# Kernel tuning notes

Measured on AMD Instinct MI355X. Metric: run time of the kernel, lower is better.

## Reference

```python
import jax, jax.numpy as jnp
import numpy as np

B, TC, TT, E, V = 512, 64, 16, 512, 256
E2 = E // 2


def entmax15(z):
    # exact sort-based 1.5-entmax over last axis (Peters et al., 2019)
    z = z / 2.0
    z = z - jnp.max(z, axis=-1, keepdims=True)  # shift-invariant, for stability
    z_srt = -jnp.sort(-z, axis=-1)
    d = z.shape[-1]
    rho = jnp.arange(1, d + 1, dtype=z.dtype)
    mean = jnp.cumsum(z_srt, axis=-1) / rho
    mean_sq = jnp.cumsum(z_srt * z_srt, axis=-1) / rho
    ss = rho * (mean_sq - mean * mean)
    delta = (1.0 - ss) / rho
    pos = delta > 0
    sqrt_d = jnp.where(pos, jnp.sqrt(jnp.where(pos, delta, 1.0)), 0.0)
    tau = mean - sqrt_d
    k = jnp.sum((tau <= z_srt).astype(jnp.int32), axis=-1, keepdims=True)
    tau_star = jnp.take_along_axis(tau, k - 1, axis=-1)
    y = jnp.clip(z - tau_star, 0.0)
    return y * y


def _mha(q_seq, kv, wq, wk, wv, bq, bk, bv, wo, bo):
    # single-head attention; q_seq: (T,B,E) decoder states, kv: (B,S,E) encoder memory
    e = q_seq.shape[-1]
    q = (q_seq @ wq.T + bq) * (1.0 / jnp.sqrt(jnp.asarray(e, q_seq.dtype)))
    k = kv @ wk.T + bk
    v = kv @ wv.T + bv
    a = jax.nn.softmax(jnp.einsum('tbe,bse->bts', q, k), axis=-1)
    o = jnp.einsum('bts,bse->tbe', a, v)
    return o @ wo.T + bo


def setup_inputs() -> dict:
    key = jax.random.key(0)
    ks = jax.random.split(key, 20)
    rn = lambda k, s, sc=1.0: sc * jax.random.normal(k, s, dtype=jnp.float32)
    z = lambda s: jnp.zeros(s, jnp.float32)
    return {
        'char_encoding': rn(ks[0], (B, TC, E)),
        'char_hn0': rn(ks[1], (B, E2)),
        'char_cn0': rn(ks[2], (B, E2)),
        'tag_encoding': rn(ks[3], (B, TT, E)),
        'tag_hn0': rn(ks[4], (B, E2)),
        'tag_cn0': rn(ks[5], (B, E2)),
        'true_output_seq': jax.random.uniform(ks[6], (B, TC, V), dtype=jnp.float32),
        'w_ih': rn(ks[7], (4 * E, V), 0.05),
        'w_hh': rn(ks[8], (4 * E, E), 0.05),
        'b_ih': z((4 * E,)),
        'b_hh': z((4 * E,)),
        'char_wq': rn(ks[9], (E, E), 0.05), 'char_wk': rn(ks[10], (E, E), 0.05), 'char_wv': rn(ks[11], (E, E), 0.05),
        'char_bq': z((E,)), 'char_bk': z((E,)), 'char_bv': z((E,)),
        'char_wo': rn(ks[12], (E, E), 0.05), 'char_bo': z((E,)),
        'tag_wq': rn(ks[13], (E, E), 0.05), 'tag_wk': rn(ks[14], (E, E), 0.05), 'tag_wv': rn(ks[15], (E, E), 0.05),
        'tag_bq': z((E,)), 'tag_bk': z((E,)), 'tag_bv': z((E,)),
        'tag_wo': rn(ks[16], (E, E), 0.05), 'tag_bo': z((E,)),
        'out_w': rn(ks[17], (V, 2 * E), 0.05),
        'out_b': z((V,)),
    }


def reference(char_encoding, char_hn0, char_cn0, tag_encoding, tag_hn0, tag_cn0, true_output_seq, w_ih, w_hh, b_ih, b_hh, char_wq, char_wk, char_wv, char_bq, char_bk, char_bv, char_wo, char_bo, tag_wq, tag_wk, tag_wv, tag_bq, tag_bk, tag_bv, tag_wo, tag_bo, out_w, out_b):
    # initial cell state = concat of the two encoders' final (h, c)
    h0 = jnp.concatenate([char_hn0, tag_hn0], axis=-1)
    c0 = jnp.concatenate([char_cn0, tag_cn0], axis=-1)
    # teacher forcing: input at t=0 is zeros, then true_output_seq[:, t]
    xs = jnp.concatenate([jnp.zeros_like(true_output_seq[:, :1]), true_output_seq[:, 1:]], axis=1)
    xs = jnp.swapaxes(xs, 0, 1)  # (T, B, V)

    def cell(carry, x):
        h, c = carry
        gates = x @ w_ih.T + b_ih + h @ w_hh.T + b_hh
        i, f, g, o = jnp.split(gates, 4, axis=-1)  # torch gate order i,f,g,o
        c = jax.nn.sigmoid(f) * c + jax.nn.sigmoid(i) * jnp.tanh(g)
        h = jax.nn.sigmoid(o) * jnp.tanh(c)
        return (h, c), h

    _, hs = jax.lax.scan(cell, (h0, c0), xs)  # (T, B, E)
    # attention queries only depend on per-step h, so batch all T queries at once
    ca = _mha(hs, char_encoding, char_wq, char_wk, char_wv, char_bq, char_bk, char_bv, char_wo, char_bo)
    ta = _mha(hs, tag_encoding, tag_wq, tag_wk, tag_wv, tag_bq, tag_bk, tag_bv, tag_wo, tag_bo)
    logits = jnp.concatenate([ca, ta], axis=-1) @ out_w.T + out_b  # (T, B, V)
    return jnp.swapaxes(entmax15(logits), 0, 1)  # (B, T, V)
```

## Files before the change

kernel.cpp:

```cpp
#include <hip/hip_runtime.h>

typedef unsigned short us;
typedef unsigned int u32;
typedef unsigned long long u64;
typedef __bf16 bf16x8 __attribute__((ext_vector_type(8)));
typedef float f32x4 __attribute__((ext_vector_type(4)));

#define MFMA(a,b,c) __builtin_amdgcn_mfma_f32_16x16x32_bf16(a,b,c,0,0,0)

__device__ __forceinline__ us f2bf(float f){
  u32 u = __builtin_bit_cast(u32, f);
  u += 0x7fffu + ((u>>16)&1u);
  return (us)(u>>16);
}
__device__ __forceinline__ float bf2f(us h){
  u32 u = ((u32)h)<<16;
  return __builtin_bit_cast(float, u);
}
__device__ __forceinline__ float sigf(float x){ return 1.0f/(1.0f+__expf(-x)); }
__device__ __forceinline__ float tanh_(float x){ float e=__expf(2.0f*x); return 1.0f - 2.0f/(e+1.0f); }


__global__ void k_prep_wperm(const float* __restrict__ w_hh, const float* __restrict__ w_ih,
                             const float* __restrict__ b_ih, const float* __restrict__ b_hh,
                             us* __restrict__ Wp, float* __restrict__ biasc){
  int n = blockIdx.x; int c = threadIdx.x;
  float v = (c < 512) ? w_hh[(size_t)n*512 + c] : w_ih[(size_t)n*256 + (c-512)];
  int g = n >> 9, eg = n & 511, eb = eg >> 4, ln = eg & 15;
  int kc = c >> 5, qd = (c >> 3) & 3, i = c & 7;
  size_t dst = ((((size_t)eb*24 + kc)*4 + g)*64 + (size_t)(qd*16 + ln))*8 + i;
  Wp[dst] = f2bf(v);
  if (c == 0) biasc[n] = b_ih[n] + b_hh[n];
}

__global__ void k_prep_state(const float* __restrict__ ch, const float* __restrict__ th,
                             const float* __restrict__ cc, const float* __restrict__ tc,
                             us* __restrict__ h0, float* __restrict__ c0){
  int i = blockIdx.x*256 + threadIdx.x;
  int b = i>>9, e = i&511;
  float hv = (e<256)? ch[b*256+e] : th[b*256+e-256];
  float cv = (e<256)? cc[b*256+e] : tc[b*256+e-256];
  h0[i] = f2bf(hv); c0[i] = cv;
}

__global__ void k_xprep(const float* __restrict__ x, us* __restrict__ xbf){
  int g = blockIdx.x*256 + threadIdx.x;
  int v0 = (g & 31) * 8;
  int b  = (g >> 5) & 511;
  int t  = g >> 14;
  const float4* src = (const float4*)(x + ((size_t)(b*64 + t))*256 + v0);
  float4 f0 = src[0], f1 = src[1];
  uint4 pk;
  pk.x = (u32)f2bf(f0.x) | ((u32)f2bf(f0.y)<<16);
  pk.y = (u32)f2bf(f0.z) | ((u32)f2bf(f0.w)<<16);
  pk.z = (u32)f2bf(f1.x) | ((u32)f2bf(f1.y)<<16);
  pk.w = (u32)f2bf(f1.z) | ((u32)f2bf(f1.w)<<16);
  *(uint4*)(xbf + ((size_t)t*512 + b)*256 + v0) = pk;
}

__global__ void k_uvec(const float* __restrict__ bq, const float* __restrict__ wk,
                       float* __restrict__ u){
  int j = blockIdx.x*128 + threadIdx.x;
  float a = 0.f;
  for (int e=0;e<512;++e) a += bq[e]*wk[(size_t)e*512 + j];
  u[j] = a;
}

__global__ void k_pvec(const float* __restrict__ wo, const float* __restrict__ bv,
                       const float* __restrict__ bo, float* __restrict__ p){
  int i = blockIdx.x*128 + threadIdx.x;
  float a = bo[i];
  for (int j=0;j<512;++j) a += wo[(size_t)i*512+j]*bv[j];
  p[i] = a;
}

__global__ void k_bc(const float* __restrict__ out_w, const float* __restrict__ pc,
                     const float* __restrict__ pt, const float* __restrict__ out_b,
                     float* __restrict__ bc){
  int v = threadIdx.x;
  float a = out_b[v];
  for (int i=0;i<512;++i) a += out_w[(size_t)v*1024+i]*pc[i];
  for (int i=0;i<512;++i) a += out_w[(size_t)v*1024+512+i]*pt[i];
  bc[v] = a;
}

template<bool TA, int OMODE>
__global__ __launch_bounds__(256) void k_pgemm(const float* __restrict__ A, int lda,
    const float* __restrict__ B, int ldb, void* C1, void* C2, int ldc, int K){
  __shared__ us As[64][40];
  __shared__ us Bs[64][40];
  int tid=threadIdx.x, w=tid>>6, lane=tid&63, qd=lane>>4, ln=lane&15;
  int m0 = blockIdx.x*64, n0 = blockIdx.y*64;
  f32x4 acc[4] = {};
  for (int kc=0; kc<K/32; ++kc){
    int k0 = kc*32;
    if (!TA){
      int r=tid>>2, c=(tid&3)*8;
      const float* ap = A + (size_t)(m0+r)*lda + k0 + c;
      float4 f0=*(const float4*)ap, f1=*(const float4*)(ap+4);
      uint4 pk;
      pk.x=(u32)f2bf(f0.x)|((u32)f2bf(f0.y)<<16);
      pk.y=(u32)f2bf(f0.z)|((u32)f2bf(f0.w)<<16);
      pk.z=(u32)f2bf(f1.x)|((u32)f2bf(f1.y)<<16);
      pk.w=(u32)f2bf(f1.z)|((u32)f2bf(f1.w)<<16);
      *(uint4*)&As[r][c] = pk;
    } else {
      int kk=tid>>3, mp=(tid&7)*8;
      const float* ap = A + (size_t)(k0+kk)*lda + m0 + mp;
      #pragma unroll
      for (int i=0;i<8;++i) As[mp+i][kk] = f2bf(ap[i]);
    }
    { int kk=tid>>3, np=(tid&7)*8;
      const float* bp = B + (size_t)(k0+kk)*ldb + n0 + np;
      #pragma unroll
      for (int i=0;i<8;++i) Bs[np+i][kk] = f2bf(bp[i]);
    }
    __syncthreads();
    bf16x8 a = *(const bf16x8*)&As[16*w+ln][qd*8];
    #pragma unroll
    for (int j=0;j<4;++j){
      bf16x8 bb = *(const bf16x8*)&Bs[16*j+ln][qd*8];
      acc[j] = MFMA(a, bb, acc[j]);
    }
    __syncthreads();
  }
  #pragma unroll
  for (int j=0;j<4;++j){
    #pragma unroll
    for (int r=0;r<4;++r){
      size_t idx = (size_t)(m0+16*w+qd*4+r)*ldc + (n0+16*j+ln);
      float v = acc[j][r];
      if (OMODE==0) ((float*)C1)[idx] = v;
      else if (OMODE==1) ((us*)C1)[idx] = f2bf(v);
      else {
        us h = f2bf(v);
        ((us*)C1)[idx] = h;
        ((us*)C2)[idx] = f2bf(v - bf2f(h));
      }
    }
  }
}

__global__ __launch_bounds__(256, 1) void k_lstm_all(
    const us* __restrict__ h0, const us* __restrict__ xbf,
    const us* __restrict__ Wp, const float* __restrict__ biasc,
    const float* __restrict__ c0, us* __restrict__ hs,
    unsigned* __restrict__ bars){
  extern __shared__ us Wf[];
  int tid = threadIdx.x, w = tid>>6, lane = tid&63, qd = lane>>4, ln = lane&15;
  int bb = blockIdx.x & 7, eb = blockIdx.x >> 3;
  int b0 = bb*64, e0 = eb*16;
  {
    const uint4* src = (const uint4*)(Wp + (size_t)eb*49152);
    uint4* dst = (uint4*)Wf;
    #pragma unroll
    for (int i=0;i<24;++i) dst[tid + 256*i] = src[tid + 256*i];
  }
  int bA = b0 + 16*w + ln;
  int bC = b0 + 16*w + qd*4;
  int e  = e0 + ln;
  float bias_[4], c_[4];
  #pragma unroll
  for (int j=0;j<4;++j) bias_[j] = biasc[j*512 + e];
  #pragma unroll
  for (int r=0;r<4;++r) c_[r] = c0[(size_t)(bC+r)*512 + e];
  __syncthreads();
  unsigned* flags = bars + (size_t)bb*512;
  unsigned* myflag = flags + eb*16;
  const unsigned* pollp = flags + (lane&31)*16;
  f32x4 xacc[4] = {};
  for (int t=0; t<64; ++t){
    if (t > 0){
      unsigned tgt = (unsigned)t;
      while (true){
        unsigned v = __hip_atomic_load(pollp, __ATOMIC_RELAXED, __HIP_MEMORY_SCOPE_AGENT);
        if (__all((int)(v >= tgt))) break;
        __builtin_amdgcn_s_sleep(1);
      }
    }
    bf16x8 afr[16];
    if (t == 0){
      const us* hrow = h0 + (size_t)bA*512;
      #pragma unroll
      for (int kc=0; kc<16; ++kc)
        afr[kc] = *(const bf16x8*)(hrow + kc*32 + qd*8);
    } else {
      const u64* hq = (const u64*)(hs + ((size_t)bA*64 + (t-1))*512);
      u64 q0[16], q1[16];
      #pragma unroll
      for (int kc=0; kc<16; ++kc){
        q0[kc] = __hip_atomic_load(hq + kc*8 + qd*2 + 0, __ATOMIC_RELAXED, __HIP_MEMORY_SCOPE_AGENT);
        q1[kc] = __hip_atomic_load(hq + kc*8 + qd*2 + 1, __ATOMIC_RELAXED, __HIP_MEMORY_SCOPE_AGENT);
      }
      #pragma unroll
      for (int kc=0; kc<16; ++kc){
        union { u64 q[2]; bf16x8 v; } u_;
        u_.q[0] = q0[kc]; u_.q[1] = q1[kc];
        afr[kc] = u_.v;
      }
    }
    f32x4 acc[4] = {xacc[0], xacc[1], xacc[2], xacc[3]};
    #pragma unroll
    for (int kc=0; kc<16; ++kc){
      #pragma unroll
      for (int j=0;j<4;++j){
        bf16x8 bfrag = *(const bf16x8*)&Wf[(size_t)((kc*4+j)*64 + lane)*8];
        acc[j] = MFMA(afr[kc], bfrag, acc[j]);
      }
    }
    us hb[4];
    #pragma unroll
    for (int r=0;r<4;++r){
      float iv = acc[0][r]+bias_[0], fv = acc[1][r]+bias_[1];
      float gv = acc[2][r]+bias_[2], ov = acc[3][r]+bias_[3];
      float cc2 = sigf(fv)*c_[r] + sigf(iv)*tanh_(gv);
      c_[r] = cc2;
      hb[r] = f2bf(sigf(ov)*tanh_(cc2));
    }
    #pragma unroll
    for (int r=0;r<4;++r){
      u32 v = hb[r];
      u32 p = v | (((u32)__shfl_xor((int)v, 1)) << 16);
      u64 q = (u64)p | (((u64)(u32)__shfl_xor((int)p, 2)) << 32);
      if ((lane & 3) == 0){
        size_t idx = ((size_t)(bC+r)*64 + t)*512 + e0 + ln;
        __hip_atomic_store((u64*)(hs + idx), q, __ATOMIC_RELAXED, __HIP_MEMORY_SCOPE_AGENT);
      }
    }
    if (t < 63){
      __syncthreads();
      if (tid == 0)
        __hip_atomic_store(myflag, (unsigned)(t+1), __ATOMIC_RELAXED, __HIP_MEMORY_SCOPE_AGENT);
      const us* xrow = xbf + ((size_t)(t+1)*512 + bA)*256;
      f32x4 xa[4] = {};
      #pragma unroll
      for (int kx=0; kx<8; ++kx){
        bf16x8 xf = *(const bf16x8*)(xrow + kx*32 + qd*8);
        #pragma unroll
        for (int j=0;j<4;++j){
          bf16x8 bfrag = *(const bf16x8*)&Wf[(size_t)(((16+kx)*4+j)*64 + lane)*8];
          xa[j] = MFMA(xf, bfrag, xa[j]);
        }
      }
      #pragma unroll
      for (int j=0;j<4;++j) xacc[j] = xa[j];
    }
  }
}

__global__ __launch_bounds__(256) void k_gemm(
    const us* __restrict__ Ap, const us* __restrict__ W,
    const float* __restrict__ bias, float alpha, us* __restrict__ C){
  __shared__ us As[128][40];
  __shared__ us Ws[128][40];
  int tid = threadIdx.x; int w = tid>>6; int lane=tid&63;
  int qd=lane>>4, ln=lane&15;
  int m0 = blockIdx.x*128, n0 = blockIdx.y*128;
  int wm = (w&1)*64, wn=(w>>1)*64;
  f32x4 acc[4][4] = {};
  int row = tid>>1; int cp = (tid&1)*16;
  for (int kc=0;kc<16;++kc){
    int k0=kc*32;
    { const uint4* ap = (const uint4*)(Ap + (size_t)(m0+row)*512 + k0+cp);
      *(uint4*)&As[row][cp]=ap[0]; *(uint4*)&As[row][cp+8]=ap[1];
    }
    { const uint4* wp = (const uint4*)(W + (size_t)(n0+row)*512 + k0+cp);
      *(uint4*)&Ws[row][cp]=wp[0]; *(uint4*)&Ws[row][cp+8]=wp[1];
    }
    __syncthreads();
    bf16x8 af[4], bfr[4];
    #pragma unroll
    for (int i=0;i<4;++i) af[i]  = *(const bf16x8*)&As[wm+16*i+ln][qd*8];
    #pragma unroll
    for (int j=0;j<4;++j) bfr[j] = *(const bf16x8*)&Ws[wn+16*j+ln][qd*8];
    #pragma unroll
    for (int i=0;i<4;++i)
      #pragma unroll
      for (int j=0;j<4;++j) acc[i][j]=MFMA(af[i],bfr[j],acc[i][j]);
    __syncthreads();
  }
  #pragma unroll
  for (int j=0;j<4;++j){
    int col = n0+wn+16*j+ln;
    float bv = bias[col];
    #pragma unroll
    for (int i=0;i<4;++i){
      #pragma unroll
      for (int r=0;r<4;++r){
        int rm = m0+wm+16*i+qd*4+r;
        C[(size_t)rm*512 + col] = f2bf(alpha*(acc[i][j][r]+bv));
      }
    }
  }
}

template<int S>
struct alignas(16) ASmem3 {
  static constexpr int SP  = (S<32)?32:S;
  static constexpr int SPp = SP+8;
  us Pbh[64][SPp];
  us Pbl[64][SPp];
  union {
    us Es[S][72];
    struct { us Eh[64][72]; us El[64][72]; } t;
  } u;
  us Ph[64][72];
  us Pl[64][72];
};

template<int S, bool ACC>
__global__ __launch_bounds__(256) void k_attn3(const us* __restrict__ hGp,
    const float* __restrict__ enc, const us* __restrict__ Mvh,
    const us* __restrict__ Mvl, float* __restrict__ out){
  constexpr int NJ  = S/16;
  constexpr int KC2 = ((S<32)?32:S)/32;
  extern __shared__ char smraw[];
  ASmem3<S>& sm = *reinterpret_cast<ASmem3<S>*>(smraw);
  int b = blockIdx.x;
  int tid=threadIdx.x, w=tid>>6, lane=tid&63, qd=lane>>4, ln=lane&15;

  f32x4 sacc[NJ];
  #pragma unroll
  for (int j=0;j<NJ;++j) sacc[j] = (f32x4){0.f,0.f,0.f,0.f};
  const us* hrow = hGp + ((size_t)(b*64 + 16*w + ln))*512;
  for (int ec=0; ec<8; ++ec){
    int e0 = ec*64;
    { int s = tid>>2, ep=(tid&3)*16;
      if (S==64 || tid < 4*S){
        const float* ap = enc + ((size_t)b*S + s)*512 + e0 + ep;
        float4 f0=*(const float4*)ap, f1=*(const float4*)(ap+4);
        float4 f2=*(const float4*)(ap+8), f3=*(const float4*)(ap+12);
        float fv[16]={f0.x,f0.y,f0.z,f0.w,f1.x,f1.y,f1.z,f1.w,
                      f2.x,f2.y,f2.z,f2.w,f3.x,f3.y,f3.z,f3.w};
        u32 pk[8];
        #pragma unroll
        for (int i=0;i<8;++i)
          pk[i] = (u32)f2bf(fv[2*i]) | ((u32)f2bf(fv[2*i+1])<<16);
        uint4* d = (uint4*)&sm.u.Es[s][ep];
        d[0] = make_uint4(pk[0],pk[1],pk[2],pk[3]);
        d[1] = make_uint4(pk[4],pk[5],pk[6],pk[7]);
      }
    }
    __syncthreads();
    #pragma unroll
    for (int kcl=0;kcl<2;++kcl){
      bf16x8 a = *(const bf16x8*)(hrow + e0 + kcl*32 + qd*8);
      #pragma unroll
      for (int j=0;j<NJ;++j){
        bf16x8 bb = *(const bf16x8*)&sm.u.Es[16*j+ln][kcl*32+qd*8];
        sacc[j] = MFMA(a, bb, sacc[j]);
      }
    }
    __syncthreads();
  }

  #pragma unroll
  for (int r=0;r<4;++r){
    float m = sacc[0][r];
    #pragma unroll
    for (int j=1;j<NJ;++j) m = fmaxf(m, sacc[j][r]);
    #pragma unroll
    for (int dl=1; dl<16; dl<<=1) m = fmaxf(m, __shfl_xor(m, dl));
    float ssum = 0.f;
    #pragma unroll
    for (int j=0;j<NJ;++j){ float e_=__expf(sacc[j][r]-m); sacc[j][r]=e_; ssum+=e_; }
    #pragma unroll
    for (int dl=1; dl<16; dl<<=1) ssum += __shfl_xor(ssum, dl);
    float inv = 1.0f/ssum;
    int R = 16*w + qd*4 + r;
    #pragma unroll
    for (int j=0;j<NJ;++j){
      float pv = sacc[j][r]*inv;
      us h = f2bf(pv);
      sm.Pbh[R][16*j+ln] = h;
      sm.Pbl[R][16*j+ln] = f2bf(pv - bf2f(h));
    }
    if (S==16){ sm.Pbh[R][16+ln]=0; sm.Pbl[R][16+ln]=0; }
  }

  f32x4 Lacc[4][4] = {};
  for (int ec=0; ec<8; ++ec){
    int e0 = ec*64;
    { int s = tid>>2, ep=(tid&3)*16;
      if (S==64 || tid < 4*S){
        const float* ap = enc + ((size_t)b*S + s)*512 + e0 + ep;
        float4 f0=*(const float4*)ap, f1=*(const float4*)(ap+4);
        float4 f2=*(const float4*)(ap+8), f3=*(const float4*)(ap+12);
        float fv[16]={f0.x,f0.y,f0.z,f0.w,f1.x,f1.y,f1.z,f1.w,
                      f2.x,f2.y,f2.z,f2.w,f3.x,f3.y,f3.z,f3.w};
        #pragma unroll
        for (int i=0;i<16;++i){
          float v = fv[i]; us h = f2bf(v);
          sm.u.t.Eh[ep+i][s] = h;
          sm.u.t.El[ep+i][s] = f2bf(v - bf2f(h));
        }
      } else if (S==16 && tid < 128){
        int s2 = 16 + ((tid-64)>>2);
        #pragma unroll
        for (int i=0;i<16;++i){ sm.u.t.Eh[ep+i][s2]=0; sm.u.t.El[ep+i][s2]=0; }
      }
    }
    __syncthreads();
    f32x4 pacc[4] = {};
    #pragma unroll
    for (int kcl=0;kcl<KC2;++kcl){
      bf16x8 ah = *(const bf16x8*)&sm.Pbh[16*w+ln][kcl*32+qd*8];
      bf16x8 al = *(const bf16x8*)&sm.Pbl[16*w+ln][kcl*32+qd*8];
      #pragma unroll
      for (int j=0;j<4;++j){
        bf16x8 bh = *(const bf16x8*)&sm.u.t.Eh[16*j+ln][kcl*32+qd*8];
        bf16x8 bl = *(const bf16x8*)&sm.u.t.El[16*j+ln][kcl*32+qd*8];
        pacc[j] = MFMA(ah, bh, pacc[j]);
        pacc[j] = MFMA(ah, bl, pacc[j]);
        pacc[j] = MFMA(al, bh, pacc[j]);
      }
    }
    #pragma unroll
    for (int j=0;j<4;++j)
      #pragma unroll
      for (int r=0;r<4;++r){
        float v = pacc[j][r]; us h = f2bf(v);
        sm.Ph[16*w+qd*4+r][16*j+ln] = h;
        sm.Pl[16*w+qd*4+r][16*j+ln] = f2bf(v - bf2f(h));
      }
    __syncthreads();
    #pragma unroll
    for (int kcl=0;kcl<2;++kcl){
      bf16x8 ah[4], al[4];
      #pragma unroll
      for (int i=0;i<4;++i){
        ah[i] = *(const bf16x8*)&sm.Ph[16*i+ln][kcl*32+qd*8];
        al[i] = *(const bf16x8*)&sm.Pl[16*i+ln][kcl*32+qd*8];
      }
      #pragma unroll
      for (int j=0;j<4;++j){
        int v = 64*w + 16*j + ln;
        bf16x8 mh = *(const bf16x8*)(Mvh + (size_t)v*512 + e0 + kcl*32 + qd*8);
        bf16x8 ml = *(const bf16x8*)(Mvl + (size_t)v*512 + e0 + kcl*32 + qd*8);
        #pragma unroll
        for (int i=0;i<4;++i){
          Lacc[i][j] = MFMA(ah[i], mh, Lacc[i][j]);
          Lacc[i][j] = MFMA(ah[i], ml, Lacc[i][j]);
          Lacc[i][j] = MFMA(al[i], mh, Lacc[i][j]);
        }
      }
    }
  }
  #pragma unroll
  for (int i=0;i<4;++i){
    #pragma unroll
    for (int j=0;j<4;++j){
      int v = 64*w + 16*j + ln;
      #pragma unroll
      for (int r=0;r<4;++r){
        size_t addr = ((size_t)b*64 + 16*i + qd*4 + r)*256 + v;
        if (ACC) out[addr] += Lacc[i][j][r];
        else     out[addr]  = Lacc[i][j][r];
      }
    }
  }
}

__global__ __launch_bounds__(256) void k_entmax(float* __restrict__ out,
                                                const float* __restrict__ bc){
  int tid=threadIdx.x; int w=tid>>6; int lane=tid&63;
  float4 bcv = *(const float4*)(bc + lane*4);
  int base = blockIdx.x*16 + w*4;
  for (int i=0;i<4;++i){
    int row = base + i;
    float* rp = out + (size_t)row*256 + lane*4;
    float4 d = *(const float4*)rp;
    float z[4] = {0.5f*(d.x+bcv.x), 0.5f*(d.y+bcv.y), 0.5f*(d.z+bcv.z), 0.5f*(d.w+bcv.w)};
    float m = fmaxf(fmaxf(z[0],z[1]), fmaxf(z[2],z[3]));
    #pragma unroll
    for (int dl=1; dl<64; dl<<=1) m = fmaxf(m, __shfl_xor(m, dl));
    #pragma unroll
    for (int k=0;k<4;++k) z[k] -= m;
    float tau = -1.0f;
    for (int it=0; it<14; ++it){
      float s1=0.f, s2=0.f;
      #pragma unroll
      for (int k=0;k<4;++k){
        float dd = z[k]-tau; dd = fmaxf(dd, 0.f);
        s1 += dd; s2 += dd*dd;
      }
      #pragma unroll
      for (int dl=1; dl<64; dl<<=1){ s1 += __shfl_xor(s1, dl); s2 += __shfl_xor(s2, dl); }
      tau += (s2 - 1.0f) / (2.0f*fmaxf(s1, 1e-12f));
    }
    float4 y;
    { float dd;
      dd = fmaxf(z[0]-tau,0.f); y.x = dd*dd;
      dd = fmaxf(z[1]-tau,0.f); y.y = dd*dd;
      dd = fmaxf(z[2]-tau,0.f); y.z = dd*dd;
      dd = fmaxf(z[3]-tau,0.f); y.w = dd*dd;
    }
    *(float4*)rp = y;
  }
}


extern "C" void kernel_launch(void* const* d_in, const int* in_sizes, int n_in,
                              void* d_out, int out_size, void* d_ws, size_t ws_size,
                              hipStream_t stream){
  (void)in_sizes; (void)n_in; (void)out_size; (void)ws_size;
  const float* char_enc = (const float*)d_in[0];
  const float* char_hn0 = (const float*)d_in[1];
  const float* char_cn0 = (const float*)d_in[2];
  const float* tag_enc  = (const float*)d_in[3];
  const float* tag_hn0  = (const float*)d_in[4];
  const float* tag_cn0  = (const float*)d_in[5];
  const float* true_out = (const float*)d_in[6];
  const float* w_ih = (const float*)d_in[7];
  const float* w_hh = (const float*)d_in[8];
  const float* b_ih = (const float*)d_in[9];
  const float* b_hh = (const float*)d_in[10];
  const float* c_wq = (const float*)d_in[11];
  const float* c_wk = (const float*)d_in[12];
  const float* c_wv = (const float*)d_in[13];
  const float* c_bq = (const float*)d_in[14];
  const float* c_bv = (const float*)d_in[16];
  const float* c_wo = (const float*)d_in[17];
  const float* c_bo = (const float*)d_in[18];
  const float* t_wq = (const float*)d_in[19];
  const float* t_wk = (const float*)d_in[20];
  const float* t_wv = (const float*)d_in[21];
  const float* t_bq = (const float*)d_in[22];
  const float* t_bv = (const float*)d_in[24];
  const float* t_wo = (const float*)d_in[25];
  const float* t_bo = (const float*)d_in[26];
  const float* out_w = (const float*)d_in[27];
  const float* out_b = (const float*)d_in[28];
  float* out = (float*)d_out;

  char* base = (char*)d_ws;
  char* regA = base;
  us*    Wp    = (us*)   (regA + 0);
  float* biasc = (float*)(regA + 3145728);
  us*    h0    = (us*)   (regA + 3153920);
  float* cst   = (float*)(regA + 3678208);
  float* M1f   = (float*)(regA + 4726784);
  float* M2f   = (float*)(regA + 5251072);
  us*    xbf   = (us*)   (regA + 5775360);
  us*    hG    = (us*)   regA;
  char* regB = base + 33554432;
  us*    Gc_w  = (us*)(regB + 0);
  us*    Gt_w  = (us*)(regB + 524288);
  us*    M1vh  = (us*)(regB + 1048576);
  us*    M1vl  = (us*)(regB + 1310720);
  us*    M2vh  = (us*)(regB + 1572864);
  us*    M2vl  = (us*)(regB + 1835008);
  float* u_c   = (float*)(regB + 2097152);
  float* u_t   = (float*)(regB + 2099200);
  float* p_c   = (float*)(regB + 2101248);
  float* p_t   = (float*)(regB + 2103296);
  float* bc    = (float*)(regB + 2105344);
  us*    hs    = (us*)(base + 33554432 + 2106368);
  unsigned* bars = (unsigned*)(base + 33554432 + 2106368 + 33554432);

  static bool attr_done = false;
  if (!attr_done){
    hipFuncSetAttribute(reinterpret_cast<const void*>(&k_lstm_all),
                        hipFuncAttributeMaxDynamicSharedMemorySize, 131072);
    attr_done = true;
  }

  hipMemsetAsync(bars, 0, 16384, stream);
  k_prep_wperm<<<2048, 768, 0, stream>>>(w_hh, w_ih, b_ih, b_hh, Wp, biasc);
  k_prep_state<<<1024, 256, 0, stream>>>(char_hn0, tag_hn0, char_cn0, tag_cn0, h0, cst);
  k_xprep<<<4096, 256, 0, stream>>>(true_out, xbf);
  k_pgemm<true,1><<<dim3(8,8),256,0,stream>>>(c_wk, 512, c_wq, 512, Gc_w, nullptr, 512, 512);
  k_pgemm<true,1><<<dim3(8,8),256,0,stream>>>(t_wk, 512, t_wq, 512, Gt_w, nullptr, 512, 512);
  k_pgemm<false,0><<<dim3(4,8),256,0,stream>>>(out_w,     1024, c_wo, 512, M1f, nullptr, 512, 512);
  k_pgemm<false,0><<<dim3(4,8),256,0,stream>>>(out_w+512, 1024, t_wo, 512, M2f, nullptr, 512, 512);
  k_pgemm<false,2><<<dim3(4,8),256,0,stream>>>(M1f, 512, c_wv, 512, M1vh, M1vl, 512, 512);
  k_pgemm<false,2><<<dim3(4,8),256,0,stream>>>(M2f, 512, t_wv, 512, M2vh, M2vl, 512, 512);
  k_uvec<<<4,128,0,stream>>>(c_bq, c_wk, u_c);
  k_uvec<<<4,128,0,stream>>>(t_bq, t_wk, u_t);
  k_pvec<<<4,128,0,stream>>>(c_wo, c_bv, c_bo, p_c);
  k_pvec<<<4,128,0,stream>>>(t_wo, t_bv, t_bo, p_t);
  k_bc<<<1,256,0,stream>>>(out_w, p_c, p_t, out_b, bc);

  k_lstm_all<<<256, 256, 98304, stream>>>(h0, xbf, Wp, biasc, cst, hs, bars);

  const float scale = 0.044194173824159216f;
  k_gemm<<<dim3(256,4),256,0,stream>>>(hs, Gc_w, u_c, scale, hG);
  k_attn3<64,false><<<512,256,sizeof(ASmem3<64>),stream>>>(hG, char_enc, M1vh, M1vl, out);
  k_gemm<<<dim3(256,4),256,0,stream>>>(hs, Gt_w, u_t, scale, hG);
  k_attn3<16,true ><<<512,256,sizeof(ASmem3<16>),stream>>>(hG, tag_enc, M2vh, M2vl, out);
  k_entmax<<<2048,256,0,stream>>>(out, bc);
}
```

Baseline: 1.121 ms.

## Parallelize bias-vector kernels and use plain loads when LSTM group shares an XCC

Replaces the serial single-thread-per-output bias precompute kernels (uvec, pvec, bc) with split-K atomic and wave-reduction versions that use many more blocks and coalesced float4 loads. In the persistent LSTM kernel, each block publishes its XCC id. If all blocks in a batch group sit on the same XCC, the hidden-state exchange uses ordinary loads and stores instead of agent-scope atomics, which are meant to cost more. The risk is coherence: plain loads may hit stale L2/L1 data if the same-XCC assumption or the cache behaviour does not hold. It also adds a start-up handshake and an extra memset.

```diff
diff --git a/kernel.cpp b/kernel.cpp
--- a/kernel.cpp
+++ b/kernel.cpp
@@ -58,30 +58,51 @@
   *(uint4*)(xbf + ((size_t)t*512 + b)*256 + v0) = pk;
 }
 
-__global__ void k_uvec(const float* __restrict__ bq, const float* __restrict__ wk,
-                       float* __restrict__ u){
-  int j = blockIdx.x*128 + threadIdx.x;
+__global__ void k_uvec2(const float* __restrict__ bq, const float* __restrict__ wk,
+                        float* __restrict__ u){
+  int j = blockIdx.x*256 + threadIdx.x;
+  int e0 = blockIdx.y*64;
   float a = 0.f;
-  for (int e=0;e<512;++e) a += bq[e]*wk[(size_t)e*512 + j];
-  u[j] = a;
-}
-
-__global__ void k_pvec(const float* __restrict__ wo, const float* __restrict__ bv,
-                       const float* __restrict__ bo, float* __restrict__ p){
-  int i = blockIdx.x*128 + threadIdx.x;
-  float a = bo[i];
-  for (int j=0;j<512;++j) a += wo[(size_t)i*512+j]*bv[j];
-  p[i] = a;
-}
-
-__global__ void k_bc(const float* __restrict__ out_w, const float* __restrict__ pc,
-                     const float* __restrict__ pt, const float* __restrict__ out_b,
-                     float* __restrict__ bc){
-  int v = threadIdx.x;
-  float a = out_b[v];
-  for (int i=0;i<512;++i) a += out_w[(size_t)v*1024+i]*pc[i];
-  for (int i=0;i<512;++i) a += out_w[(size_t)v*1024+512+i]*pt[i];
-  bc[v] = a;
+  #pragma unroll 8
+  for (int e=e0; e<e0+64; ++e) a += bq[e]*wk[(size_t)e*512 + j];
+  atomicAdd(u+j, a);
+}
+
+__global__ __launch_bounds__(256) void k_pvec2(const float* __restrict__ wo,
+    const float* __restrict__ bv, const float* __restrict__ bo, float* __restrict__ p){
+  int w = threadIdx.x>>6, lane = threadIdx.x&63;
+  int i = blockIdx.x*4 + w;
+  const float4* wr = (const float4*)(wo + (size_t)i*512);
+  const float4* bvv = (const float4*)bv;
+  float a = 0.f;
+  #pragma unroll
+  for (int k=0;k<2;++k){
+    float4 x = wr[lane*2+k];
+    float4 y = bvv[lane*2+k];
+    a += x.x*y.x + x.y*y.y + x.z*y.z + x.w*y.w;
+  }
+  #pragma unroll
+  for (int dl=1; dl<64; dl<<=1) a += __shfl_xor(a, dl);
+  if (lane==0) p[i] = a + bo[i];
+}
+
+__global__ __launch_bounds__(256) void k_bc2(const float* __restrict__ out_w,
+    const float* __restrict__ pc, const float* __restrict__ pt,
+    const float* __restrict__ out_b, float* __restrict__ bc){
+  int w = threadIdx.x>>6, lane = threadIdx.x&63;
+  int v = blockIdx.x*4 + w;
+  const float4* wr = (const float4*)(out_w + (size_t)v*1024);
+  float a = 0.f;
+  #pragma unroll
+  for (int k=0;k<4;++k){
+    float4 x = wr[lane*4+k];
+    int base = (lane*4+k)*4;
+    const float* pv = (base < 512) ? (pc + base) : (pt + (base-512));
+    a += x.x*pv[0] + x.y*pv[1] + x.z*pv[2] + x.w*pv[3];
+  }
+  #pragma unroll
+  for (int dl=1; dl<64; dl<<=1) a += __shfl_xor(a, dl);
+  if (lane==0) bc[v] = a + out_b[v];
 }
 
 template<bool TA, int OMODE>
@@ -150,6 +171,13 @@
   int tid = threadIdx.x, w = tid>>6, lane = tid&63, qd = lane>>4, ln = lane&15;
   int bb = blockIdx.x & 7, eb = blockIdx.x >> 3;
   int b0 = bb*64, e0 = eb*16;
+
+  u32 myxcc = 0;
+  asm volatile("s_getreg_b32 %0, hwreg(HW_REG_XCC_ID)" : "=s"(myxcc));
+  unsigned* xcds = bars + 4096 + (size_t)bb*512;
+  if (tid == 0)
+    __hip_atomic_store(xcds + eb*16, myxcc + 1u, __ATOMIC_RELAXED, __HIP_MEMORY_SCOPE_AGENT);
+
   {
     const uint4* src = (const uint4*)(Wp + (size_t)eb*49152);
     uint4* dst = (uint4*)Wf;
@@ -165,6 +193,20 @@
   #pragma unroll
   for (int r=0;r<4;++r) c_[r] = c0[(size_t)(bC+r)*512 + e];
   __syncthreads();
+
+  bool fast;
+  {
+    const unsigned* xp = xcds + (lane&31)*16;
+    u32 ids;
+    while (true){
+      ids = __hip_atomic_load(xp, __ATOMIC_RELAXED, __HIP_MEMORY_SCOPE_AGENT);
+      if (__all((int)(ids != 0))) break;
+      __builtin_amdgcn_s_sleep(8);
+    }
+    u32 id0 = (u32)__shfl((int)ids, 0);
+    fast = __all((int)(ids == id0));
+  }
+
   unsigned* flags = bars + (size_t)bb*512;
   unsigned* myflag = flags + eb*16;
   const unsigned* pollp = flags + (lane&31)*16;
@@ -177,10 +219,16 @@
         if (__all((int)(v >= tgt))) break;
         __builtin_amdgcn_s_sleep(1);
       }
+      asm volatile("" ::: "memory");
     }
     bf16x8 afr[16];
     if (t == 0){
       const us* hrow = h0 + (size_t)bA*512;
+      #pragma unroll
+      for (int kc=0; kc<16; ++kc)
+        afr[kc] = *(const bf16x8*)(hrow + kc*32 + qd*8);
+    } else if (fast){
+      const us* hrow = hs + ((size_t)bA*64 + (t-1))*512;
       #pragma unroll
       for (int kc=0; kc<16; ++kc)
         afr[kc] = *(const bf16x8*)(hrow + kc*32 + qd*8);
@@ -224,7 +272,10 @@
       u64 q = (u64)p | (((u64)(u32)__shfl_xor((int)p, 2)) << 32);
       if ((lane & 3) == 0){
         size_t idx = ((size_t)(bC+r)*64 + t)*512 + e0 + ln;
-        __hip_atomic_store((u64*)(hs + idx), q, __ATOMIC_RELAXED, __HIP_MEMORY_SCOPE_AGENT);
+        if (fast)
+          *(u64*)(hs + idx) = q;
+        else
+          __hip_atomic_store((u64*)(hs + idx), q, __ATOMIC_RELAXED, __HIP_MEMORY_SCOPE_AGENT);
       }
     }
     if (t < 63){
@@ -565,7 +616,8 @@
     attr_done = true;
   }
 
-  hipMemsetAsync(bars, 0, 16384, stream);
+  hipMemsetAsync(bars, 0, 32768, stream);
+  hipMemsetAsync(u_c, 0, 4096, stream);
   k_prep_wperm<<<2048, 768, 0, stream>>>(w_hh, w_ih, b_ih, b_hh, Wp, biasc);
   k_prep_state<<<1024, 256, 0, stream>>>(char_hn0, tag_hn0, char_cn0, tag_cn0, h0, cst);
   k_xprep<<<4096, 256, 0, stream>>>(true_out, xbf);
@@ -575,11 +627,11 @@
   k_pgemm<false,0><<<dim3(4,8),256,0,stream>>>(out_w+512, 1024, t_wo, 512, M2f, nullptr, 512, 512);
   k_pgemm<false,2><<<dim3(4,8),256,0,stream>>>(M1f, 512, c_wv, 512, M1vh, M1vl, 512, 512);
   k_pgemm<false,2><<<dim3(4,8),256,0,stream>>>(M2f, 512, t_wv, 512, M2vh, M2vl, 512, 512);
-  k_uvec<<<4,128,0,stream>>>(c_bq, c_wk, u_c);
-  k_uvec<<<4,128,0,stream>>>(t_bq, t_wk, u_t);
-  k_pvec<<<4,128,0,stream>>>(c_wo, c_bv, c_bo, p_c);
-  k_pvec<<<4,128,0,stream>>>(t_wo, t_bv, t_bo, p_t);
-  k_bc<<<1,256,0,stream>>>(out_w, p_c, p_t, out_b, bc);
+  k_uvec2<<<dim3(2,8),256,0,stream>>>(c_bq, c_wk, u_c);
+  k_uvec2<<<dim3(2,8),256,0,stream>>>(t_bq, t_wk, u_t);
+  k_pvec2<<<128,256,0,stream>>>(c_wo, c_bv, c_bo, p_c);
+  k_pvec2<<<128,256,0,stream>>>(t_wo, t_bv, t_bo, p_t);
+  k_bc2<<<64,256,0,stream>>>(out_w, p_c, p_t, out_b, bc);
 
   k_lstm_all<<<256, 256, 98304, stream>>>(h0, xbf, Wp, biasc, cst, hs, bars);
 
```

New measurement: 963.7 us. -14.0%, faster.
